# Kernel tuning notes

Measured on AMD Instinct MI355X. Metric: run time of the kernel, lower is better.

## Reference

```python
import jax, jax.numpy as jnp
import numpy as np

N_NODES = 100000
N_EDGES = 800000
NUM_FEATURES = 81
NUM_BOND = 22
OUT_CHANNEL = 64
D_COORD = 3  # 'distance' rule applies to feature indices [0:3]


def setup_inputs() -> dict:
    key = jax.random.key(0)
    k1, k2, k3, k4, k5, k6 = jax.random.split(key, 6)
    features = jax.random.normal(k1, (N_NODES, NUM_FEATURES), dtype=jnp.float32)
    bond = jax.random.normal(k2, (N_EDGES, NUM_BOND), dtype=jnp.float32)
    w_s = jax.random.normal(k3, (NUM_FEATURES, OUT_CHANNEL), dtype=jnp.float32) * 0.1
    w_n = jax.random.normal(k4, (NUM_FEATURES + NUM_BOND, OUT_CHANNEL), dtype=jnp.float32) * 0.1
    src = jax.random.randint(k5, (N_EDGES,), 0, N_NODES)
    dst = jax.random.randint(k6, (N_EDGES,), 0, N_NODES)
    return {"features": features, "bond": bond, "w_s": w_s, "w_n": w_n,
            "src": src, "dst": dst}


def reference(features, bond, w_s, w_n, src, dst):
    # Gather endpoint features per edge: [E, F]
    self_f = features[src]
    nbr_f = features[dst]

    # Rule 1: 'distance' on [0:3] -> keep neighbour coords, compute L2 distance
    diff = self_f[:, :D_COORD] - nbr_f[:, :D_COORD]
    dist = jnp.sqrt(jnp.sum(diff * diff, axis=-1))      # [E]
    d = jnp.where(dist > 0, dist, jnp.float32(0.01))

    # Rule 2 (last, single-index): 'sum' on [3:]
    seg1 = nbr_f[:, :D_COORD]                           # [E, 3]
    seg2 = self_f[:, D_COORD:] + nbr_f[:, D_COORD:]     # [E, 78]

    # Distance normalization applies to the whole combined vector (pre-bond)
    combined = jnp.concatenate([seg1, seg2], axis=-1) / (d * d)[:, None]
    edge_vec = jnp.concatenate([combined, bond], axis=-1)  # [E, F + B]

    contrib = edge_vec @ w_n                            # [E, out]
    agg = jax.ops.segment_sum(contrib, src, num_segments=features.shape[0])
    return features @ w_s + agg                         # [N, out]
```

## Files before the change

### kernel.cpp

```cpp
#include <hip/hip_runtime.h>

#define N_NODES 100000
#define N_EDGES 800000
#define NF 81
#define NB 22
#define OC 64
#define SCAN_CHUNK 1024
#define SCAN_BLOCKS ((N_NODES + SCAN_CHUNK - 1) / SCAN_CHUNK)

typedef __attribute__((ext_vector_type(8))) short bf16x8;
typedef __attribute__((ext_vector_type(4))) float f32x4;

#if defined(__has_builtin)
#if __has_builtin(__builtin_amdgcn_fdot2_f32_bf16)
#define HAVE_FDOT2 1
#endif
#endif

#ifdef HAVE_FDOT2
typedef __attribute__((ext_vector_type(2))) __bf16 bfv2;
#endif

__device__ inline float dot2b(unsigned a, unsigned b, float c) {
#ifdef HAVE_FDOT2
    return __builtin_amdgcn_fdot2_f32_bf16(__builtin_bit_cast(bfv2, a),
                                           __builtin_bit_cast(bfv2, b), c, false);
#else
    return c + __uint_as_float(a << 16)         * __uint_as_float(b << 16)
             + __uint_as_float(a & 0xffff0000u) * __uint_as_float(b & 0xffff0000u);
#endif
}

__device__ inline unsigned short bfsplit(float v, float& rest) {
    const unsigned b = __float_as_uint(v);
    const unsigned short h = (unsigned short)((b + 0x7fffu + ((b >> 16) & 1u)) >> 16);
    rest = v - __uint_as_float(((unsigned)h) << 16);
    return h;
}

__global__ void k_wprep(const float* __restrict__ w_s, const float* __restrict__ w_n,
                        short* __restrict__ bt)
{
    const int tid = blockIdx.x * blockDim.x + threadIdx.x;
    if (tid >= 128 * 96) return;
    const int c = tid / 96;
    const int k = tid - c * 96;
    float v = 0.f;
    if (k < NF) v = (c < OC) ? w_s[k * OC + c] : w_n[k * OC + (c - OC)];
    float rest, dummy;
    const unsigned short h = bfsplit(v, rest);
    const unsigned short l = bfsplit(rest, dummy);
    bt[c * 96 + k]               = (short)h;
    bt[128 * 96 + c * 96 + k]    = (short)l;
}

__global__ __launch_bounds__(256) void k_node_mfma(
    const float* __restrict__ feat, const short* __restrict__ bt,
    float* __restrict__ out, float* __restrict__ pb, float4* __restrict__ xyz)
{
    __shared__ short shA[2 * 64 * 104];
    const int t    = threadIdx.x;
    const int lane = t & 63;
    const int w    = t >> 6;
    const int n0   = blockIdx.x * 64;

    const int krow = (lane >> 4) * 8;
    bf16x8 Bh[3][2], Bl[3][2];
#pragma unroll
    for (int kt = 0; kt < 3; ++kt)
#pragma unroll
        for (int c = 0; c < 2; ++c) {
            const int col = w * 32 + c * 16 + (lane & 15);
            const int off = col * 96 + kt * 32 + krow;
            Bh[kt][c] = *(const bf16x8*)(bt + off);
            Bl[kt][c] = *(const bf16x8*)(bt + 128 * 96 + off);
        }

    const long gbase = (long)n0 * NF;
    const long gmax  = (long)N_NODES * NF;
    for (int j = t; j < (64 * NF) / 4; j += 256) {
        const int flat = j * 4;
        float v[4];
        if (gbase + flat + 3 < gmax) {
            const float4 q = *(const float4*)(feat + gbase + flat);
            v[0] = q.x; v[1] = q.y; v[2] = q.z; v[3] = q.w;
        } else {
#pragma unroll
            for (int i = 0; i < 4; ++i)
                v[i] = (gbase + flat + i < gmax) ? feat[gbase + flat + i] : 0.f;
        }
#pragma unroll
        for (int i = 0; i < 4; ++i) {
            const int fi  = flat + i;
            const int row = (int)((unsigned)fi / 81u);
            const int k   = fi - row * 81;
            float rest, dummy;
            const unsigned short h = bfsplit(v[i], rest);
            const unsigned short l = bfsplit(rest, dummy);
            shA[row * 104 + k]        = (short)h;
            shA[6656 + row * 104 + k] = (short)l;
        }
    }
    for (int j = t; j < 64 * 16; j += 256) {
        const int row = j >> 4, k = NF + (j & 15);
        shA[row * 104 + k] = 0;
        shA[6656 + row * 104 + k] = 0;
    }

    if (t < 64 && n0 + t < N_NODES) {
        const float* fp = feat + (long)(n0 + t) * NF;
        xyz[n0 + t] = make_float4(fp[0], fp[1], fp[2], 0.f);
    }
    __syncthreads();

    f32x4 acc[4][2];
#pragma unroll
    for (int rt = 0; rt < 4; ++rt)
#pragma unroll
        for (int c = 0; c < 2; ++c)
            acc[rt][c] = (f32x4){0.f, 0.f, 0.f, 0.f};

#pragma unroll
    for (int kt = 0; kt < 3; ++kt) {
        bf16x8 Ah[4], Al[4];
#pragma unroll
        for (int rt = 0; rt < 4; ++rt) {
            const int o = (rt * 16 + (lane & 15)) * 104 + kt * 32 + krow;
            Ah[rt] = *(const bf16x8*)(shA + o);
            Al[rt] = *(const bf16x8*)(shA + 6656 + o);
        }
#pragma unroll
        for (int rt = 0; rt < 4; ++rt)
#pragma unroll
            for (int c = 0; c < 2; ++c) {
                f32x4 a = acc[rt][c];
                a = __builtin_amdgcn_mfma_f32_16x16x32_bf16(Ah[rt], Bh[kt][c], a, 0, 0, 0);
                a = __builtin_amdgcn_mfma_f32_16x16x32_bf16(Ah[rt], Bl[kt][c], a, 0, 0, 0);
                a = __builtin_amdgcn_mfma_f32_16x16x32_bf16(Al[rt], Bh[kt][c], a, 0, 0, 0);
                acc[rt][c] = a;
            }
    }

    const int c0    = w * 32 + (lane & 15);
    float* db       = (w < 2) ? out : pb;
    const int cbase = (w < 2) ? c0 : c0 - OC;
    const int r0    = (lane >> 4) * 4;
#pragma unroll
    for (int rt = 0; rt < 4; ++rt)
#pragma unroll
        for (int c = 0; c < 2; ++c)
#pragma unroll
            for (int reg = 0; reg < 4; ++reg) {
                const int node = n0 + rt * 16 + r0 + reg;
                if (node < N_NODES)
                    db[(long)node * OC + cbase + c * 16] = acc[rt][c][reg];
            }
}

__global__ void k_hist(const int* __restrict__ src, int* __restrict__ cnt,
                       int* __restrict__ rank) {
    const int e = blockIdx.x * blockDim.x + threadIdx.x;
    if (e < N_EDGES) rank[e] = atomicAdd(&cnt[src[e]], 1);
}

__global__ __launch_bounds__(256) void k_scan_blk(
    const int* __restrict__ cnt, int* __restrict__ row, int* __restrict__ bsum)
{
    __shared__ int sh[256];
    const int t = threadIdx.x;
    const int base = blockIdx.x * SCAN_CHUNK + t * 4;
    int c0 = 0, c1 = 0, c2 = 0, c3 = 0;
    if (base + 3 < N_NODES) {
        const int4 c = *(const int4*)(cnt + base);
        c0 = c.x; c1 = c.y; c2 = c.z; c3 = c.w;
    } else {
        if (base + 0 < N_NODES) c0 = cnt[base + 0];
        if (base + 1 < N_NODES) c1 = cnt[base + 1];
        if (base + 2 < N_NODES) c2 = cnt[base + 2];
    }
    const int s = c0 + c1 + c2 + c3;
    sh[t] = s;
    __syncthreads();
    for (int off = 1; off < 256; off <<= 1) {
        int v = sh[t];
        int a = (t >= off) ? sh[t - off] : 0;
        __syncthreads();
        sh[t] = v + a;
        __syncthreads();
    }
    const int excl = sh[t] - s;
    if (t == 255) bsum[blockIdx.x] = sh[255];
    if (base + 3 < N_NODES) {
        int4 r;
        r.x = excl; r.y = excl + c0; r.z = excl + c0 + c1; r.w = excl + c0 + c1 + c2;
        *(int4*)(row + base) = r;
    } else {
        int e = excl;
        if (base + 0 < N_NODES) { row[base + 0] = e; e += c0; }
        if (base + 1 < N_NODES) { row[base + 1] = e; e += c1; }
        if (base + 2 < N_NODES) { row[base + 2] = e; }
    }
}

__global__ void k_scan_top(int* __restrict__ bsum, int* __restrict__ row) {
    __shared__ int sh[128];
    const int t = threadIdx.x;
    const int v = (t < SCAN_BLOCKS) ? bsum[t] : 0;
    sh[t] = v;
    __syncthreads();
    for (int off = 1; off < 128; off <<= 1) {
        int x = sh[t];
        int a = (t >= off) ? sh[t - off] : 0;
        __syncthreads();
        sh[t] = x + a;
        __syncthreads();
    }
    if (t < SCAN_BLOCKS) bsum[t] = sh[t] - v;
    if (t == 127) row[N_NODES] = sh[127];
}

__global__ __launch_bounds__(256) void k_scan_add(
    int* __restrict__ row, const int* __restrict__ bsum)
{
    const int off = bsum[blockIdx.x];
    const int base = blockIdx.x * SCAN_CHUNK + threadIdx.x * 4;
    if (base + 3 < N_NODES) {
        int4 r = *(const int4*)(row + base);
        r.x += off; r.y += off; r.z += off; r.w += off;
        *(int4*)(row + base) = r;
    } else {
#pragma unroll
        for (int k = 0; k < 4; ++k)
            if (base + k < N_NODES)
                row[base + k] += off;
    }
}

__global__ void k_perm(const int* __restrict__ src, const int* __restrict__ rank,
                       const int* __restrict__ row, int* __restrict__ perm) {
    const int e = blockIdx.x * blockDim.x + threadIdx.x;
    if (e < N_EDGES) perm[row[src[e]] + rank[e]] = e;
}

__device__ inline unsigned pk_bf16(float a, float b) {
    const unsigned ua = (__float_as_uint(a) + 0x8000u) >> 16;
    const unsigned ub = (__float_as_uint(b) + 0x8000u) & 0xffff0000u;
    return ua | ub;
}

__global__ __launch_bounds__(256) void k_prep(
    const int* __restrict__ src, const int* __restrict__ dst,
    const float* __restrict__ bond, const float4* __restrict__ xyz,
    unsigned* __restrict__ recA, unsigned* __restrict__ recB)
{
    const int e = blockIdx.x * blockDim.x + threadIdx.x;
    if (e >= N_EDGES) return;
    const int s = src[e];
    const int d = dst[e];
    const float4 a = xyz[s], b = xyz[d];
    const float dx = a.x - b.x, dy = a.y - b.y, dz = a.z - b.z;
    const float d2 = dx * dx + dy * dy + dz * dz;
    const float inv = (d2 > 0.f) ? __builtin_amdgcn_rcpf(d2) : 1.0e4f;

    float2 bv[11];
    const float2* bp = (const float2*)(bond + (long)e * NB);
#pragma unroll
    for (int j = 0; j < 11; ++j) bv[j] = bp[j];

    unsigned p[11];
#pragma unroll
    for (int j = 0; j < 11; ++j) p[j] = pk_bf16(bv[j].x, bv[j].y);

    unsigned* r = recA + (size_t)e * 12;
    *(uint4*)(r)     = make_uint4(p[0], p[1], p[2], p[3]);
    *(uint4*)(r + 4) = make_uint4(p[4], p[5], p[6], p[7]);
    *(uint4*)(r + 8) = make_uint4(p[8], p[9], p[10], __float_as_uint(inv));
    recB[e] = (unsigned)d;
}

__global__ __launch_bounds__(256) void k_gather(
    const int* __restrict__ row, const int* __restrict__ perm,
    const unsigned* __restrict__ recA, const unsigned* __restrict__ recB,
    const float* __restrict__ w_n, const float* __restrict__ pb,
    const float4* __restrict__ xyz, float* __restrict__ out)
{
    const int lane = threadIdx.x & 63;
    const int wid  = (int)((blockIdx.x * blockDim.x + threadIdx.x) >> 6);
    if (wid >= N_NODES) return;
    const int n = __builtin_amdgcn_readfirstlane(wid);

    unsigned wp[11];
#pragma unroll
    for (int j = 0; j < 11; ++j)
        wp[j] = pk_bf16(w_n[(NF + 2 * j) * OC + lane],
                        w_n[(NF + 2 * j + 1) * OC + lane]);
    const float w0 = w_n[0 * OC + lane];
    const float w1 = w_n[1 * OC + lane];
    const float w2 = w_n[2 * OC + lane];

    const int rs = row[n], re = row[n + 1];
    const float4 xs = xyz[n];
    const float pa = pb[(long)n * OC + lane]
                   - (xs.x * w0 + xs.y * w1 + xs.z * w2);

    float acc = 0.f;
    int i = rs;

    for (; i + 4 <= re; i += 4) {
        int pe[4];
#pragma unroll
        for (int u = 0; u < 4; ++u)
            pe[u] = __builtin_amdgcn_readfirstlane(perm[i + u]);
        unsigned P[4][12];
        unsigned db[4];
#pragma unroll
        for (int u = 0; u < 4; ++u) {
            const unsigned* r = recA + (size_t)pe[u] * 12;
#pragma unroll
            for (int j = 0; j < 12; ++j) P[u][j] = r[j];
            db[u] = recB[pe[u]];
        }
        float pbt[4];
#pragma unroll
        for (int u = 0; u < 4; ++u)
            pbt[u] = pb[(long)(int)db[u] * OC + lane];
        float c[4];
#pragma unroll
        for (int u = 0; u < 4; ++u)
            c[u] = __uint_as_float(P[u][11]) * (pa + pbt[u]);
#pragma unroll
        for (int j = 0; j < 11; ++j)
#pragma unroll
            for (int u = 0; u < 4; ++u)
                c[u] = dot2b(P[u][j], wp[j], c[u]);
        acc += (c[0] + c[1]) + (c[2] + c[3]);
    }

    for (; i < re; ++i) {
        const int pe = __builtin_amdgcn_readfirstlane(perm[i]);
        const unsigned* r = recA + (size_t)pe * 12;
        unsigned p[12];
#pragma unroll
        for (int j = 0; j < 12; ++j) p[j] = r[j];
        const unsigned dbt = recB[pe];
        const float pbt = pb[(long)(int)dbt * OC + lane];
        float c = __uint_as_float(p[11]) * (pa + pbt);
#pragma unroll
        for (int j = 0; j < 11; ++j)
            c = dot2b(p[j], wp[j], c);
        acc += c;
    }

    out[(long)n * OC + lane] += acc;
}

extern "C" void kernel_launch(void* const* d_in, const int* in_sizes, int n_in,
                              void* d_out, int out_size, void* d_ws, size_t ws_size,
                              hipStream_t stream) {
    const float* feat = (const float*)d_in[0];
    const float* bond = (const float*)d_in[1];
    const float* w_s  = (const float*)d_in[2];
    const float* w_n  = (const float*)d_in[3];
    const int*   src  = (const int*)d_in[4];
    const int*   dstv = (const int*)d_in[5];
    float* out = (float*)d_out;

    char* base = (char*)d_ws;
    float*    pb     = (float*)   (base);
    float4*   xyz    = (float4*)  (base + 25600000);
    int*      row    = (int*)     (base + 27200000);
    int*      cnt    = (int*)     (base + 27600016);
    int*      rank   = (int*)     (base + 28000016);
    int*      bsum   = (int*)     (base + 31200016);
    unsigned* recA   = (unsigned*)(base + 31200640);
    unsigned* recB   = (unsigned*)(base + 69600640);
    int*      perm   = (int*)     (base + 72800640);
    short*    btw    = (short*)recA;

    hipMemsetAsync(cnt, 0, N_NODES * sizeof(int), stream);

    k_wprep   <<<48, 256, 0, stream>>>(w_s, w_n, btw);
    k_node_mfma<<<(N_NODES + 63) / 64, 256, 0, stream>>>(feat, btw, out, pb, xyz);
    k_prep    <<<(N_EDGES + 255) / 256, 0 ? 0 : 256, 0, stream>>>(src, dstv, bond,
                                                                  xyz, recA, recB);
    k_hist    <<<(N_EDGES + 255) / 256, 256, 0, stream>>>(src, cnt, rank);
    k_scan_blk<<<SCAN_BLOCKS, 256, 0, stream>>>(cnt, row, bsum);
    k_scan_top<<<1, 128, 0, stream>>>(bsum, row);
    k_scan_add<<<SCAN_BLOCKS, 256, 0, stream>>>(row, bsum);
    k_perm    <<<(N_EDGES + 255) / 256, 256, 0, stream>>>(src, rank, row, perm);
    k_gather  <<<(N_NODES * 64 + 255) / 256, 256, 0, stream>>>(row, perm, recA,
                                                               recB, w_n, pb,
                                                               xyz, out);
}
```

Measured before the change: 330.7 us.

## Aggregate bond features per node before projecting, shrink per-edge records

Because the bond term is linear and not scaled by the distance factor, a new per-node kernel first sums each node's incoming bond vectors in fp32 and packs them to bf16. The gather kernel then does a single 11-term dot per node instead of one per edge. Per-edge records shrink from 48+4 bytes to an 8-byte (inverse distance, dst) pair, and pa*inv is factored out as pa*sum(inv). This removes most per-edge dot work and record traffic, at the cost of an extra launch whose scattered bond-row reads use only 11 of 64 lanes per wave.

```diff
diff --git a/kernel.cpp b/kernel.cpp
--- a/kernel.cpp
+++ b/kernel.cpp
@@ -36,6 +36,16 @@
     const unsigned short h = (unsigned short)((b + 0x7fffu + ((b >> 16) & 1u)) >> 16);
     rest = v - __uint_as_float(((unsigned)h) << 16);
     return h;
+}
+
+__device__ inline unsigned pk_bf16(float a, float b) {
+    const unsigned ua = (__float_as_uint(a) + 0x8000u) >> 16;
+    const unsigned ub = (__float_as_uint(b) + 0x8000u) & 0xffff0000u;
+    return ua | ub;
+}
+
+__device__ inline int clampe(int p) {
+    return ((unsigned)p < (unsigned)N_EDGES) ? p : 0;
 }
 
 __global__ void k_wprep(const float* __restrict__ w_s, const float* __restrict__ w_n,
@@ -242,16 +252,8 @@
     if (e < N_EDGES) perm[row[src[e]] + rank[e]] = e;
 }
 
-__device__ inline unsigned pk_bf16(float a, float b) {
-    const unsigned ua = (__float_as_uint(a) + 0x8000u) >> 16;
-    const unsigned ub = (__float_as_uint(b) + 0x8000u) & 0xffff0000u;
-    return ua | ub;
-}
-
-__global__ __launch_bounds__(256) void k_prep(
-    const int* __restrict__ src, const int* __restrict__ dst,
-    const float* __restrict__ bond, const float4* __restrict__ xyz,
-    unsigned* __restrict__ recA, unsigned* __restrict__ recB)
+__global__ void k_prep8(const int* __restrict__ src, const int* __restrict__ dst,
+                        const float4* __restrict__ xyz, uint2* __restrict__ rec8)
 {
     const int e = blockIdx.x * blockDim.x + threadIdx.x;
     if (e >= N_EDGES) return;
@@ -261,26 +263,49 @@
     const float dx = a.x - b.x, dy = a.y - b.y, dz = a.z - b.z;
     const float d2 = dx * dx + dy * dy + dz * dz;
     const float inv = (d2 > 0.f) ? __builtin_amdgcn_rcpf(d2) : 1.0e4f;
-
-    float2 bv[11];
-    const float2* bp = (const float2*)(bond + (long)e * NB);
-#pragma unroll
-    for (int j = 0; j < 11; ++j) bv[j] = bp[j];
-
-    unsigned p[11];
-#pragma unroll
-    for (int j = 0; j < 11; ++j) p[j] = pk_bf16(bv[j].x, bv[j].y);
-
-    unsigned* r = recA + (size_t)e * 12;
-    *(uint4*)(r)     = make_uint4(p[0], p[1], p[2], p[3]);
-    *(uint4*)(r + 4) = make_uint4(p[4], p[5], p[6], p[7]);
-    *(uint4*)(r + 8) = make_uint4(p[8], p[9], p[10], __float_as_uint(inv));
-    recB[e] = (unsigned)d;
+    rec8[e] = make_uint2(__float_as_uint(inv), (unsigned)d);
+}
+
+__global__ __launch_bounds__(256) void k_bsum(
+    const int* __restrict__ row, const int* __restrict__ perm,
+    const float* __restrict__ bond, unsigned* __restrict__ bs)
+{
+    const int lane = threadIdx.x & 63;
+    const int wid  = (int)((blockIdx.x * blockDim.x + threadIdx.x) >> 6);
+    if (wid >= N_NODES) return;
+    const int n = __builtin_amdgcn_readfirstlane(wid);
+    const int rs = row[n], re = row[n + 1];
+
+    float sx = 0.f, sy = 0.f;
+    int i = rs;
+    for (; i + 4 <= re; i += 4) {
+        int pe[4];
+#pragma unroll
+        for (int u = 0; u < 4; ++u)
+            pe[u] = __builtin_amdgcn_readfirstlane(clampe(perm[i + u]));
+        if (lane < 11) {
+            float2 v[4];
+#pragma unroll
+            for (int u = 0; u < 4; ++u)
+                v[u] = *(const float2*)(bond + (size_t)pe[u] * NB + 2 * lane);
+#pragma unroll
+            for (int u = 0; u < 4; ++u) { sx += v[u].x; sy += v[u].y; }
+        }
+    }
+    for (; i < re; ++i) {
+        const int pe = __builtin_amdgcn_readfirstlane(clampe(perm[i]));
+        if (lane < 11) {
+            const float2 v = *(const float2*)(bond + (size_t)pe * NB + 2 * lane);
+            sx += v.x; sy += v.y;
+        }
+    }
+    if (lane < 11)
+        bs[n * 12 + lane] = pk_bf16(sx, sy);
 }
 
 __global__ __launch_bounds__(256) void k_gather(
     const int* __restrict__ row, const int* __restrict__ perm,
-    const unsigned* __restrict__ recA, const unsigned* __restrict__ recB,
+    const uint2* __restrict__ rec8, const unsigned* __restrict__ bs,
     const float* __restrict__ w_n, const float* __restrict__ pb,
     const float4* __restrict__ xyz, float* __restrict__ out)
 {
@@ -304,54 +329,44 @@
                    - (xs.x * w0 + xs.y * w1 + xs.z * w2);
 
     float acc = 0.f;
+    float inv_sum = 0.f;
     int i = rs;
 
-    for (; i + 4 <= re; i += 4) {
-        int pe[4];
-#pragma unroll
-        for (int u = 0; u < 4; ++u)
-            pe[u] = __builtin_amdgcn_readfirstlane(perm[i + u]);
-        unsigned P[4][12];
-        unsigned db[4];
-#pragma unroll
-        for (int u = 0; u < 4; ++u) {
-            const unsigned* r = recA + (size_t)pe[u] * 12;
-#pragma unroll
-            for (int j = 0; j < 12; ++j) P[u][j] = r[j];
-            db[u] = recB[pe[u]];
-        }
-        float pbt[4];
-#pragma unroll
-        for (int u = 0; u < 4; ++u)
-            pbt[u] = pb[(long)(int)db[u] * OC + lane];
-        float c[4];
-#pragma unroll
-        for (int u = 0; u < 4; ++u)
-            c[u] = __uint_as_float(P[u][11]) * (pa + pbt[u]);
-#pragma unroll
-        for (int j = 0; j < 11; ++j)
-#pragma unroll
-            for (int u = 0; u < 4; ++u)
-                c[u] = dot2b(P[u][j], wp[j], c[u]);
-        acc += (c[0] + c[1]) + (c[2] + c[3]);
-    }
-
+    for (; i + 8 <= re; i += 8) {
+        int pe[8];
+#pragma unroll
+        for (int u = 0; u < 8; ++u)
+            pe[u] = __builtin_amdgcn_readfirstlane(clampe(perm[i + u]));
+        uint2 r[8];
+#pragma unroll
+        for (int u = 0; u < 8; ++u) r[u] = rec8[pe[u]];
+        float pbt[8];
+#pragma unroll
+        for (int u = 0; u < 8; ++u)
+            pbt[u] = pb[(long)(int)r[u].y * OC + lane];
+#pragma unroll
+        for (int u = 0; u < 8; ++u) {
+            const float inv = __uint_as_float(r[u].x);
+            acc += inv * pbt[u];
+            inv_sum += inv;
+        }
+    }
     for (; i < re; ++i) {
-        const int pe = __builtin_amdgcn_readfirstlane(perm[i]);
-        const unsigned* r = recA + (size_t)pe * 12;
-        unsigned p[12];
-#pragma unroll
-        for (int j = 0; j < 12; ++j) p[j] = r[j];
-        const unsigned dbt = recB[pe];
-        const float pbt = pb[(long)(int)dbt * OC + lane];
-        float c = __uint_as_float(p[11]) * (pa + pbt);
-#pragma unroll
-        for (int j = 0; j < 11; ++j)
-            c = dot2b(p[j], wp[j], c);
-        acc += c;
-    }
-
-    out[(long)n * OC + lane] += acc;
+        const int pe = __builtin_amdgcn_readfirstlane(clampe(perm[i]));
+        const uint2 r = rec8[pe];
+        const float inv = __uint_as_float(r.x);
+        acc += inv * pb[(long)(int)r.y * OC + lane];
+        inv_sum += inv;
+    }
+    acc += pa * inv_sum;
+
+    const unsigned* bsn = bs + n * 12;
+    float bc = 0.f;
+#pragma unroll
+    for (int j = 0; j < 11; ++j)
+        bc = dot2b(bsn[j], wp[j], bc);
+
+    out[(long)n * OC + lane] += acc + bc;
 }
 
 extern "C" void kernel_launch(void* const* d_in, const int* in_sizes, int n_in,
@@ -371,24 +386,24 @@
     int*      row    = (int*)     (base + 27200000);
     int*      cnt    = (int*)     (base + 27600016);
     int*      rank   = (int*)     (base + 28000016);
-    int*      bsum   = (int*)     (base + 31200016);
-    unsigned* recA   = (unsigned*)(base + 31200640);
-    unsigned* recB   = (unsigned*)(base + 69600640);
-    int*      perm   = (int*)     (base + 72800640);
-    short*    btw    = (short*)recA;
+    int*      bsc    = (int*)     (base + 31200016);
+    short*    btw    = (short*)   (base + 31200640);
+    uint2*    rec8   = (uint2*)   (base + 31249792);
+    int*      perm   = (int*)     (base + 37649792);
+    unsigned* bsv    = (unsigned*)(base + 40849792);
 
     hipMemsetAsync(cnt, 0, N_NODES * sizeof(int), stream);
 
     k_wprep   <<<48, 256, 0, stream>>>(w_s, w_n, btw);
     k_node_mfma<<<(N_NODES + 63) / 64, 256, 0, stream>>>(feat, btw, out, pb, xyz);
-    k_prep    <<<(N_EDGES + 255) / 256, 0 ? 0 : 256, 0, stream>>>(src, dstv, bond,
-                                                                  xyz, recA, recB);
     k_hist    <<<(N_EDGES + 255) / 256, 256, 0, stream>>>(src, cnt, rank);
-    k_scan_blk<<<SCAN_BLOCKS, 256, 0, stream>>>(cnt, row, bsum);
-    k_scan_top<<<1, 128, 0, stream>>>(bsum, row);
-    k_scan_add<<<SCAN_BLOCKS, 256, 0, stream>>>(row, bsum);
+    k_scan_blk<<<SCAN_BLOCKS, 256, 0, stream>>>(cnt, row, bsc);
+    k_scan_top<<<1, 128, 0, stream>>>(bsc, row);
+    k_scan_add<<<SCAN_BLOCKS, 256, 0, stream>>>(row, bsc);
     k_perm    <<<(N_EDGES + 255) / 256, 256, 0, stream>>>(src, rank, row, perm);
-    k_gather  <<<(N_NODES * 64 + 255) / 256, 256, 0, stream>>>(row, perm, recA,
-                                                               recB, w_n, pb,
+    k_prep8   <<<(N_EDGES + 255) / 256, 256, 0, stream>>>(src, dstv, xyz, rec8);
+    k_bsum    <<<(N_NODES * 64 + 255) / 256, 256, 0, stream>>>(row, perm, bond, bsv);
+    k_gather  <<<(N_NODES * 64 + 255) / 256, 256, 0, stream>>>(row, perm, rec8,
+                                                               bsv, w_n, pb,
                                                                xyz, out);
 }
```

Result: no change. 334.1 us (+1.0%).
